# Kernel tuning notes

Hardware: AMD Instinct MI355X
Metric: run time of the kernel (lower is better)

## Reference

```python
import jax, jax.numpy as jnp
import numpy as np

B_BOX, N_CLASS = 2, 20          # B, C from __init__
LAMBDA_C, LAMBDA_N = 5.0, 0.5   # self.lambda_c, self.lambda_n
GRID = 49                        # hard-coded 7x7 grid


def setup_inputs() -> dict:
    key = jax.random.key(0)
    k1, k2 = jax.random.split(key)
    outputs = jax.random.uniform(k1, (16384, GRID, 5 * B_BOX + N_CLASS), dtype=jnp.float32)
    target = jax.random.uniform(k2, (16384, 10, 5), dtype=jnp.float32)
    return {"outputs": outputs, "target": target}


def _forward(outputs, target):
    batch, n_obj = target.shape[0], target.shape[1]
    Bb = B_BOX
    # --- target preprocessing: sqrt(w,h), nan -> -1 ---
    tgt = target.at[:, :, 2:4].set(jnp.sqrt(target[:, :, 2:4]))
    tgt = jnp.nan_to_num(tgt, nan=-1.0)
    # --- grid-cell assignment (vectorized version of the batch*obj python loop) ---
    x, y = tgt[:, :, 0], tgt[:, :, 1]
    xi = jnp.trunc(7.0 * x).astype(jnp.int32)   # int(7*x) truncation semantics
    yi = jnp.trunc(7.0 * y).astype(jnp.int32)
    cell = jnp.clip(7 * yi + xi, 0, GRID - 1)
    valid = ((x != -1.0) & (xi >= 0)).astype(tgt.dtype)
    sel = jax.nn.one_hot(cell, GRID, dtype=tgt.dtype) * valid[..., None]   # [b,obj,49]
    ti = sel[:, :, :, None] * tgt[:, :, None, :]                           # [b,obj,49,5]
    ti = jnp.transpose(ti, (0, 2, 1, 3))                                   # [b,49,obj,5]
    # --- permute: move first Bb nonzero boxes of each cell to the top ---
    nonzero = jnp.sum(ti, axis=-1) > 0                                     # [b,49,obj]
    slot = jnp.cumsum(nonzero.astype(jnp.int32), axis=-1) - 1
    slot = jnp.where(nonzero, jnp.minimum(slot, Bb), Bb)                   # Bb = discard slot
    oh = jax.nn.one_hot(slot, Bb + 1, dtype=ti.dtype)                      # [b,49,obj,Bb+1]
    gt = jnp.einsum('bcos,bcod->bcsd', oh, ti)[:, :, :Bb]                  # [b,49,Bb,5]
    # --- iou_matrix (boxes stored as center +/- (sqrt_wh)^2 corners) ---
    pred5 = outputs[:, :, :5 * Bb].reshape(batch, GRID, Bb, 5)
    pdims = pred5[..., :4]
    pdims = pdims.at[..., 2:4].set(jnp.sqrt(pdims[..., 2:4]))
    gdims = gt[..., :4]
    gmin, gmax = gdims[..., :2] - gdims[..., 2:4] ** 2, gdims[..., :2] + gdims[..., 2:4] ** 2
    pmin, pmax = pdims[..., :2] - pdims[..., 2:4] ** 2, pdims[..., :2] + pdims[..., 2:4] ** 2
    # pairwise: axis2 = pred box, axis3 = gt box
    imin = jnp.maximum(gmin[:, :, None, :, :], pmin[:, :, :, None, :])
    imax = jnp.minimum(gmax[:, :, None, :, :], pmax[:, :, :, None, :])
    d = jnp.maximum(imax - imin, 0.0)
    inter = d[..., 0] * d[..., 1]                                          # [b,49,Bb,Bb]
    gwh, pwh = jnp.abs(gmax - gmin), jnp.abs(pmax - pmin)
    garea = (gwh[..., 0] * gwh[..., 1])[:, :, None, :]
    parea = (pwh[..., 0] * pwh[..., 1])[:, :, :, None]
    union = garea + parea - inter
    iou = jnp.where(union == 0, 0.0, inter / jnp.where(union == 0, 1.0, union))  # nan_to_num(i/u)
    t_index = jnp.argmax(iou, axis=2)                                      # [b,49,Bb]
    # --- construct_model_ground_truth: gather assigned gt box + truncated-int confidence ---
    idx = jnp.broadcast_to(t_index[..., None], gt.shape)
    gathered = jnp.take_along_axis(gt, idx, axis=2)                        # [b,49,Bb,5]
    r1wh, r2wh = pred5[..., 2:4] ** 2, gathered[..., 2:4] ** 2
    min1, max1 = pred5[..., :2] - 0.5 * r1wh, pred5[..., :2] + 0.5 * r1wh
    min2, max2 = gathered[..., :2] - 0.5 * r2wh, gathered[..., :2] + 0.5 * r2wh
    d2 = jnp.maximum(jnp.minimum(max1, max2) - jnp.maximum(min1, min2), 0.0)
    inter2 = d2[..., 0] * d2[..., 1]
    union2 = r1wh[..., 0] * r1wh[..., 1] + r2wh[..., 0] * r2wh[..., 1] - inter2
    conf = jnp.where((jnp.trunc(union2) == 0) | (jnp.trunc(inter2) == 0), 0.0,
                     jnp.trunc(inter2 / jnp.where(union2 == 0, 1.0, union2)))
    final_gt = gathered.at[..., 4].set(conf)
    # --- obj loss: lambda_c on x,y,w,h; 1.0 on confidence ---
    w = jnp.array([LAMBDA_C, LAMBDA_C, LAMBDA_C, LAMBDA_C, 1.0], dtype=outputs.dtype)
    obj_loss = jnp.sum(w * (final_gt - pred5) ** 2)
    # --- noobj loss (faithfully replicates original bug: mask is recreated per loop
    #     iteration, so only the last (batch, bbox) iteration's mask survives) ---
    pconf, gconf = pred5[..., 4], final_gt[..., 4]                         # [b,49,Bb]
    mask = jnp.ones_like(gconf)
    mask = mask.at[batch - 1, jnp.arange(GRID), t_index[batch - 1, :, Bb - 1]].set(0.0)
    noobj_loss = LAMBDA_N * jnp.sum(((pconf - gconf) * mask) ** 2)
    # --- class loss ---
    cls_scores = outputs[:, :, 5 * Bb:]                                    # [b,49,C]
    max_pred = jnp.max(cls_scores, axis=2)[..., None]                      # [b,49,1]
    pred_cls = jnp.argmax(cls_scores, axis=2)[..., None]                   # [b,49,1]
    predictions = max_pred * pconf                                         # [b,49,Bb]
    truths = (final_gt[..., 4] == pred_cls.astype(outputs.dtype)).astype(outputs.dtype)
    cell_mask = jnp.sign(jnp.sum(final_gt, axis=-1))                       # [b,49,Bb]
    class_loss = jnp.sum(cell_mask * (truths - predictions) ** 2)
    return (obj_loss + noobj_loss + class_loss) / batch


def reference(outputs, target):
    return _forward(outputs, target)
```

## Files before the change

### kernel.cpp

```cpp
#include <hip/hip_runtime.h>
#include <math.h>

#define GRID_CELLS 49
#define NOBJ 10
#define BB 2
#define NCLS 20
#define OUT_C 30
#define LAMBDA_C 5.0f
#define LAMBDA_N 0.5f
#define BLOCK 256

__global__ __launch_bounds__(BLOCK) void yolo_loss_flat(
    const float* __restrict__ outputs,
    const float* __restrict__ target,
    float* __restrict__ partial,
    int batch)
{
    const int gid = blockIdx.x * BLOCK + threadIdx.x;
    const int total = batch * GRID_CELLS;
    float lsum = 0.0f;

    if (gid < total) {
        const int b = gid / GRID_CELLS;
        const int c = gid - b * GRID_CELLS;

        float tv[NOBJ * 5];
        {
            const float2* t2 = reinterpret_cast<const float2*>(target + (size_t)b * (NOBJ * 5));
            #pragma unroll
            for (int i = 0; i < (NOBJ * 5) / 2; ++i) {
                float2 v = t2[i];
                tv[2 * i]     = v.x;
                tv[2 * i + 1] = v.y;
            }
        }
        float g0[5] = {0.f, 0.f, 0.f, 0.f, 0.f};
        float g1[5] = {0.f, 0.f, 0.f, 0.f, 0.f};
        int cnt = 0;
        #pragma unroll
        for (int o = 0; o < NOBJ; ++o) {
            float t0 = tv[o * 5 + 0];
            float t1 = tv[o * 5 + 1];
            float t2 = sqrtf(tv[o * 5 + 2]);
            float t3 = sqrtf(tv[o * 5 + 3]);
            float t4 = tv[o * 5 + 4];
            if (t0 != t0) t0 = -1.0f;
            if (t1 != t1) t1 = -1.0f;
            if (t2 != t2) t2 = -1.0f;
            if (t3 != t3) t3 = -1.0f;
            if (t4 != t4) t4 = -1.0f;
            int xi = (int)truncf(7.0f * t0);
            int yi = (int)truncf(7.0f * t1);
            int cell = 7 * yi + xi;
            cell = cell < 0 ? 0 : (cell > GRID_CELLS - 1 ? GRID_CELLS - 1 : cell);
            bool valid = (t0 != -1.0f) && (xi >= 0);
            float s5 = t0 + t1 + t2 + t3 + t4;
            bool nz = valid && (s5 > 0.0f);
            if (nz && cell == c) {
                if (cnt == 0) { g0[0]=t0; g0[1]=t1; g0[2]=t2; g0[3]=t3; g0[4]=t4; }
                else if (cnt == 1) { g1[0]=t0; g1[1]=t1; g1[2]=t2; g1[3]=t3; g1[4]=t4; }
                ++cnt;
            }
        }
        float g[BB][5];
        #pragma unroll
        for (int d = 0; d < 5; ++d) { g[0][d] = g0[d]; g[1][d] = g1[d]; }

        float vals[OUT_C];
        {
            const float2* r2 = reinterpret_cast<const float2*>(outputs + (size_t)gid * OUT_C);
            #pragma unroll
            for (int i = 0; i < OUT_C / 2; ++i) {
                float2 v = r2[i];
                vals[2 * i]     = v.x;
                vals[2 * i + 1] = v.y;
            }
        }
        float pred[BB][5];
        #pragma unroll
        for (int p = 0; p < BB; ++p)
            #pragma unroll
            for (int d = 0; d < 5; ++d) pred[p][d] = vals[p * 5 + d];

        float pminx[BB], pmaxx[BB], pminy[BB], pmaxy[BB], parea[BB];
        #pragma unroll
        for (int p = 0; p < BB; ++p) {
            float sw = sqrtf(pred[p][2]);
            float sh = sqrtf(pred[p][3]);
            float w2 = sw * sw, h2 = sh * sh;
            pminx[p] = pred[p][0] - w2; pmaxx[p] = pred[p][0] + w2;
            pminy[p] = pred[p][1] - h2; pmaxy[p] = pred[p][1] + h2;
            parea[p] = fabsf(pmaxx[p] - pminx[p]) * fabsf(pmaxy[p] - pminy[p]);
        }
        float gminx[BB], gmaxx[BB], gminy[BB], gmaxy[BB], garea[BB];
        #pragma unroll
        for (int s = 0; s < BB; ++s) {
            float w2 = g[s][2] * g[s][2], h2 = g[s][3] * g[s][3];
            gminx[s] = g[s][0] - w2; gmaxx[s] = g[s][0] + w2;
            gminy[s] = g[s][1] - h2; gmaxy[s] = g[s][1] + h2;
            garea[s] = fabsf(gmaxx[s] - gminx[s]) * fabsf(gmaxy[s] - gminy[s]);
        }
        int t_index[BB];
        #pragma unroll
        for (int s = 0; s < BB; ++s) {
            float best = 0.0f; int bi = 0;
            #pragma unroll
            for (int p = 0; p < BB; ++p) {
                float ix0 = fmaxf(gminx[s], pminx[p]);
                float iy0 = fmaxf(gminy[s], pminy[p]);
                float ix1 = fminf(gmaxx[s], pmaxx[p]);
                float iy1 = fminf(gmaxy[s], pmaxy[p]);
                float dx = fmaxf(ix1 - ix0, 0.0f);
                float dy = fmaxf(iy1 - iy0, 0.0f);
                float inter = dx * dy;
                float uni = garea[s] + parea[p] - inter;
                float iou = (uni == 0.0f) ? 0.0f : inter / uni;
                if (p == 0) { best = iou; bi = 0; }
                else if (iou > best) { best = iou; bi = p; }
            }
            t_index[s] = bi;
        }
        float maxp = vals[5 * BB]; int cls = 0;
        #pragma unroll
        for (int k = 1; k < NCLS; ++k) {
            float v = vals[5 * BB + k];
            if (v > maxp) { maxp = v; cls = k; }
        }
        float fcls = (float)cls;

        #pragma unroll
        for (int s = 0; s < BB; ++s) {
            float ga[5];
            #pragma unroll
            for (int d = 0; d < 5; ++d) ga[d] = (t_index[s] == 0) ? g[0][d] : g[1][d];
            float r1w = pred[s][2] * pred[s][2], r1h = pred[s][3] * pred[s][3];
            float r2w = ga[2] * ga[2],           r2h = ga[3] * ga[3];
            float min1x = pred[s][0] - 0.5f * r1w, max1x = pred[s][0] + 0.5f * r1w;
            float min1y = pred[s][1] - 0.5f * r1h, max1y = pred[s][1] + 0.5f * r1h;
            float min2x = ga[0] - 0.5f * r2w, max2x = ga[0] + 0.5f * r2w;
            float min2y = ga[1] - 0.5f * r2h, max2y = ga[1] + 0.5f * r2h;
            float dx = fmaxf(fminf(max1x, max2x) - fmaxf(min1x, min2x), 0.0f);
            float dy = fmaxf(fminf(max1y, max2y) - fmaxf(min1y, min2y), 0.0f);
            float inter2 = dx * dy;
            float uni2 = r1w * r1h + r2w * r2h - inter2;
            float conf;
            if (truncf(uni2) == 0.0f || truncf(inter2) == 0.0f) conf = 0.0f;
            else conf = truncf(inter2 / (uni2 == 0.0f ? 1.0f : uni2));
            #pragma unroll
            for (int d = 0; d < 4; ++d) {
                float df = ga[d] - pred[s][d];
                lsum += LAMBDA_C * df * df;
            }
            { float df = conf - pred[s][4]; lsum += df * df; }
            float m = 1.0f;
            if (b == batch - 1 && s == t_index[BB - 1]) m = 0.0f;
            float dn = (pred[s][4] - conf) * m;
            lsum += LAMBDA_N * dn * dn;
            float predn = maxp * pred[s][4];
            float truth = (conf == fcls) ? 1.0f : 0.0f;
            float sum5 = ga[0] + ga[1] + ga[2] + ga[3] + conf;
            float cm = (sum5 > 0.0f) ? 1.0f : ((sum5 < 0.0f) ? -1.0f : 0.0f);
            float dcl = truth - predn;
            lsum += cm * dcl * dcl;
        }
    }

    #pragma unroll
    for (int off = 32; off > 0; off >>= 1) lsum += __shfl_down(lsum, off, 64);
    __shared__ float red[BLOCK / 64];
    const int wid = threadIdx.x >> 6;
    const int lane = threadIdx.x & 63;
    if (lane == 0) red[wid] = lsum;
    __syncthreads();
    if (threadIdx.x == 0) {
        float s = 0.0f;
        #pragma unroll
        for (int w = 0; w < BLOCK / 64; ++w) s += red[w];
        partial[blockIdx.x] = s;
    }
}

__global__ __launch_bounds__(256) void reduce_partials(
    const float* __restrict__ partial, int n, float* __restrict__ out, float inv_batch)
{
    float s = 0.0f;
    for (int i = threadIdx.x; i < n; i += 256) s += partial[i];
    #pragma unroll
    for (int off = 32; off > 0; off >>= 1) s += __shfl_down(s, off, 64);
    __shared__ float red[4];
    const int wid = threadIdx.x >> 6;
    const int lane = threadIdx.x & 63;
    if (lane == 0) red[wid] = s;
    __syncthreads();
    if (threadIdx.x == 0) out[0] = (red[0] + red[1] + red[2] + red[3]) * inv_batch;
}

extern "C" void kernel_launch(void* const* d_in, const int* in_sizes, int n_in,
                              void* d_out, int out_size, void* d_ws, size_t ws_size,
                              hipStream_t stream) {
    const float* outputs = (const float*)d_in[0];
    const float* target  = (const float*)d_in[1];
    float* out = (float*)d_out;
    float* partial = (float*)d_ws;
    int batch = in_sizes[1] / (NOBJ * 5);
    int total = batch * GRID_CELLS;
    int nblocks = (total + BLOCK - 1) / BLOCK;
    yolo_loss_flat<<<nblocks, BLOCK, 0, stream>>>(outputs, target, partial, batch);
    reduce_partials<<<1, 256, 0, stream>>>(partial, nblocks, out, 1.0f / (float)batch);
}
```

Baseline: 153.1 us.

## Stream target and output loads, add occupancy hint, replace reduce kernel with atomics

Target and output rows are now consumed as they are loaded instead of being staged into large register arrays. This cuts register pressure, and a launch_bounds hint asks for four blocks per CU to raise occupancy. The second reduction kernel is dropped: each block atomically adds its scaled partial into the output, which is zeroed first by a memset. This saves a kernel launch, but the float sum order becomes nondeterministic and about 3136 atomics contend on a single address.

```diff
diff --git a/kernel.cpp b/kernel.cpp
--- a/kernel.cpp
+++ b/kernel.cpp
@@ -10,77 +10,80 @@
 #define LAMBDA_N 0.5f
 #define BLOCK 256
 
-__global__ __launch_bounds__(BLOCK) void yolo_loss_flat(
+__global__ __launch_bounds__(BLOCK, 4) void yolo_loss_flat(
     const float* __restrict__ outputs,
     const float* __restrict__ target,
-    float* __restrict__ partial,
-    int batch)
+    float* __restrict__ out,
+    int batch, float inv_batch)
 {
     const int gid = blockIdx.x * BLOCK + threadIdx.x;
-    const int total = batch * GRID_CELLS;
     float lsum = 0.0f;
 
-    if (gid < total) {
+    if (gid < batch * GRID_CELLS) {
         const int b = gid / GRID_CELLS;
         const int c = gid - b * GRID_CELLS;
 
-        float tv[NOBJ * 5];
-        {
-            const float2* t2 = reinterpret_cast<const float2*>(target + (size_t)b * (NOBJ * 5));
-            #pragma unroll
-            for (int i = 0; i < (NOBJ * 5) / 2; ++i) {
-                float2 v = t2[i];
-                tv[2 * i]     = v.x;
-                tv[2 * i + 1] = v.y;
-            }
-        }
         float g0[5] = {0.f, 0.f, 0.f, 0.f, 0.f};
         float g1[5] = {0.f, 0.f, 0.f, 0.f, 0.f};
         int cnt = 0;
+        const float2* t2 = reinterpret_cast<const float2*>(target + (size_t)b * (NOBJ * 5));
         #pragma unroll
-        for (int o = 0; o < NOBJ; ++o) {
-            float t0 = tv[o * 5 + 0];
-            float t1 = tv[o * 5 + 1];
-            float t2 = sqrtf(tv[o * 5 + 2]);
-            float t3 = sqrtf(tv[o * 5 + 3]);
-            float t4 = tv[o * 5 + 4];
-            if (t0 != t0) t0 = -1.0f;
-            if (t1 != t1) t1 = -1.0f;
-            if (t2 != t2) t2 = -1.0f;
-            if (t3 != t3) t3 = -1.0f;
-            if (t4 != t4) t4 = -1.0f;
-            int xi = (int)truncf(7.0f * t0);
-            int yi = (int)truncf(7.0f * t1);
-            int cell = 7 * yi + xi;
-            cell = cell < 0 ? 0 : (cell > GRID_CELLS - 1 ? GRID_CELLS - 1 : cell);
-            bool valid = (t0 != -1.0f) && (xi >= 0);
-            float s5 = t0 + t1 + t2 + t3 + t4;
-            bool nz = valid && (s5 > 0.0f);
-            if (nz && cell == c) {
-                if (cnt == 0) { g0[0]=t0; g0[1]=t1; g0[2]=t2; g0[3]=t3; g0[4]=t4; }
-                else if (cnt == 1) { g1[0]=t0; g1[1]=t1; g1[2]=t2; g1[3]=t3; g1[4]=t4; }
-                ++cnt;
+        for (int i = 0; i < 5; ++i) {
+            float2 a0 = t2[5 * i + 0];
+            float2 a1 = t2[5 * i + 1];
+            float2 a2 = t2[5 * i + 2];
+            float2 a3 = t2[5 * i + 3];
+            float2 a4 = t2[5 * i + 4];
+            float v[10] = {a0.x, a0.y, a1.x, a1.y, a2.x, a2.y, a3.x, a3.y, a4.x, a4.y};
+            #pragma unroll
+            for (int h = 0; h < 2; ++h) {
+                float t0 = v[5 * h + 0];
+                float t1 = v[5 * h + 1];
+                float t2f = sqrtf(v[5 * h + 2]);
+                float t3f = sqrtf(v[5 * h + 3]);
+                float t4 = v[5 * h + 4];
+                if (t0 != t0)  t0  = -1.0f;
+                if (t1 != t1)  t1  = -1.0f;
+                if (t2f != t2f) t2f = -1.0f;
+                if (t3f != t3f) t3f = -1.0f;
+                if (t4 != t4)  t4  = -1.0f;
+                int xi = (int)truncf(7.0f * t0);
+                int yi = (int)truncf(7.0f * t1);
+                int cell = 7 * yi + xi;
+                cell = cell < 0 ? 0 : (cell > GRID_CELLS - 1 ? GRID_CELLS - 1 : cell);
+                bool valid = (t0 != -1.0f) && (xi >= 0);
+                float s5 = t0 + t1 + t2f + t3f + t4;
+                if (valid && (s5 > 0.0f) && cell == c) {
+                    if (cnt == 0)      { g0[0]=t0; g0[1]=t1; g0[2]=t2f; g0[3]=t3f; g0[4]=t4; }
+                    else if (cnt == 1) { g1[0]=t0; g1[1]=t1; g1[2]=t2f; g1[3]=t3f; g1[4]=t4; }
+                    ++cnt;
+                }
             }
         }
         float g[BB][5];
         #pragma unroll
         for (int d = 0; d < 5; ++d) { g[0][d] = g0[d]; g[1][d] = g1[d]; }
 
-        float vals[OUT_C];
+        const float2* r2 = reinterpret_cast<const float2*>(outputs + (size_t)gid * OUT_C);
+        float pred[BB][5];
         {
-            const float2* r2 = reinterpret_cast<const float2*>(outputs + (size_t)gid * OUT_C);
+            float2 p0 = r2[0], p1 = r2[1], p2 = r2[2], p3 = r2[3], p4 = r2[4];
+            pred[0][0] = p0.x; pred[0][1] = p0.y; pred[0][2] = p1.x; pred[0][3] = p1.y; pred[0][4] = p2.x;
+            pred[1][0] = p2.y; pred[1][1] = p3.x; pred[1][2] = p3.y; pred[1][3] = p4.x; pred[1][4] = p4.y;
+        }
+        float maxp; int cls;
+        {
+            float2 q0 = r2[5];
+            maxp = q0.x; cls = 0;
+            if (q0.y > maxp) { maxp = q0.y; cls = 1; }
             #pragma unroll
-            for (int i = 0; i < OUT_C / 2; ++i) {
-                float2 v = r2[i];
-                vals[2 * i]     = v.x;
-                vals[2 * i + 1] = v.y;
+            for (int i = 1; i < NCLS / 2; ++i) {
+                float2 q = r2[5 + i];
+                if (q.x > maxp) { maxp = q.x; cls = 2 * i; }
+                if (q.y > maxp) { maxp = q.y; cls = 2 * i + 1; }
             }
         }
-        float pred[BB][5];
-        #pragma unroll
-        for (int p = 0; p < BB; ++p)
-            #pragma unroll
-            for (int d = 0; d < 5; ++d) pred[p][d] = vals[p * 5 + d];
+        float fcls = (float)cls;
 
         float pminx[BB], pmaxx[BB], pminy[BB], pmaxy[BB], parea[BB];
         #pragma unroll
@@ -120,13 +123,6 @@
             }
             t_index[s] = bi;
         }
-        float maxp = vals[5 * BB]; int cls = 0;
-        #pragma unroll
-        for (int k = 1; k < NCLS; ++k) {
-            float v = vals[5 * BB + k];
-            if (v > maxp) { maxp = v; cls = k; }
-        }
-        float fcls = (float)cls;
 
         #pragma unroll
         for (int s = 0; s < BB; ++s) {
@@ -176,23 +172,8 @@
         float s = 0.0f;
         #pragma unroll
         for (int w = 0; w < BLOCK / 64; ++w) s += red[w];
-        partial[blockIdx.x] = s;
+        atomicAdd(out, s * inv_batch);
     }
-}
-
-__global__ __launch_bounds__(256) void reduce_partials(
-    const float* __restrict__ partial, int n, float* __restrict__ out, float inv_batch)
-{
-    float s = 0.0f;
-    for (int i = threadIdx.x; i < n; i += 256) s += partial[i];
-    #pragma unroll
-    for (int off = 32; off > 0; off >>= 1) s += __shfl_down(s, off, 64);
-    __shared__ float red[4];
-    const int wid = threadIdx.x >> 6;
-    const int lane = threadIdx.x & 63;
-    if (lane == 0) red[wid] = s;
-    __syncthreads();
-    if (threadIdx.x == 0) out[0] = (red[0] + red[1] + red[2] + red[3]) * inv_batch;
 }
 
 extern "C" void kernel_launch(void* const* d_in, const int* in_sizes, int n_in,
@@ -201,10 +182,9 @@
     const float* outputs = (const float*)d_in[0];
     const float* target  = (const float*)d_in[1];
     float* out = (float*)d_out;
-    float* partial = (float*)d_ws;
     int batch = in_sizes[1] / (NOBJ * 5);
     int total = batch * GRID_CELLS;
     int nblocks = (total + BLOCK - 1) / BLOCK;
-    yolo_loss_flat<<<nblocks, BLOCK, 0, stream>>>(outputs, target, partial, batch);
-    reduce_partials<<<1, 256, 0, stream>>>(partial, nblocks, out, 1.0f / (float)batch);
+    hipMemsetAsync(out, 0, sizeof(float), stream);
+    yolo_loss_flat<<<nblocks, BLOCK, 0, stream>>>(outputs, target, out, batch, 1.0f / (float)batch);
 }
```

Measured after the change: 158.6 us. +3.6%, slower.
